# Kernel tuning notes

Measured on AMD Instinct MI355X. Metric: run time of the kernel, lower is better.

## Reference

```python
import jax, jax.numpy as jnp
import numpy as np

N_NODES = 50000
N_EDGES = 800000
D_IN = 128
D_HID = 128
N_CLASSES = 10


def gcn_conv(x, edge_index, edge_weight, W, b):
    """PyG GCNConv with edge weights: add self-loops, symmetric deg^-1/2 norm,
    gather-scale-scatter aggregation, then bias."""
    n = x.shape[0]
    row, col = edge_index[0], edge_index[1]
    loop = jnp.arange(n)
    row = jnp.concatenate([row, loop])
    col = jnp.concatenate([col, loop])
    ew = jnp.concatenate([edge_weight, jnp.ones((n,), edge_weight.dtype)])
    # degree computed at target nodes (source_to_target flow)
    deg = jax.ops.segment_sum(ew, col, num_segments=n)
    dinv = jnp.where(deg > 0, jax.lax.rsqrt(deg), 0.0)
    norm = dinv[row] * ew * dinv[col]  # [E+N]
    xw = x @ W  # [N, D_HID] dense GEMM first (PyG order)
    msgs = norm[:, None] * xw[row]  # [E+N, D_HID] edge-wise gather+scale
    out = jax.ops.segment_sum(msgs, col, num_segments=n)  # scatter-add
    return out + b


def setup_inputs() -> dict:
    key = jax.random.key(0)
    ks = jax.random.split(key, 9)
    x = jax.random.normal(ks[0], (N_NODES, D_IN), dtype=jnp.float32)
    edge_index = jax.random.randint(ks[1], (2, N_EDGES), 0, N_NODES, dtype=jnp.int64)
    edge_attr = jax.random.uniform(ks[2], (N_EDGES,), dtype=jnp.float32)
    s1 = 1.0 / np.sqrt(D_IN)
    s2 = 1.0 / np.sqrt(D_HID)
    W1 = jax.random.uniform(ks[3], (D_IN, D_HID), minval=-s1, maxval=s1, dtype=jnp.float32)
    b1 = jnp.zeros((D_HID,), jnp.float32)
    W2 = jax.random.uniform(ks[4], (D_HID, D_HID), minval=-s2, maxval=s2, dtype=jnp.float32)
    b2 = jnp.zeros((D_HID,), jnp.float32)
    Wm = jax.random.uniform(ks[5], (D_HID, N_CLASSES), minval=-s2, maxval=s2, dtype=jnp.float32)
    bm = jax.random.uniform(ks[6], (N_CLASSES,), minval=-s2, maxval=s2, dtype=jnp.float32)
    return {"x": x, "edge_index": edge_index, "edge_attr": edge_attr,
            "W1": W1, "b1": b1, "W2": W2, "b2": b2, "Wm": Wm, "bm": bm}


def reference(x, edge_index, edge_attr, W1, b1, W2, b2, Wm, bm):
    h = jax.nn.relu(gcn_conv(x, edge_index, edge_attr, W1, b1))
    h = jax.nn.relu(gcn_conv(h, edge_index, edge_attr, W2, b2))
    # F.dropout(training=False) is identity in eval mode
    g = jnp.mean(h, axis=0)  # [D_HID] graph readout
    return g @ Wm + bm  # [N_CLASSES]
```

## Files before the change

### kernel.cpp

```cpp
#include <hip/hip_runtime.h>

#define DD 128
#define CAP 8192

typedef __attribute__((ext_vector_type(8))) short short8v;
typedef __attribute__((ext_vector_type(4))) float float4v;

__device__ inline unsigned short f2b(float f) {
    unsigned int x = __float_as_uint(f);
    return (unsigned short)((x + 0x7fffu + ((x >> 16) & 1u)) >> 16);
}
__device__ inline float blo(unsigned int u) { return __uint_as_float(u << 16); }
__device__ inline float bhi(unsigned int u) { return __uint_as_float(u & 0xffff0000u); }

__global__ void wconv2_kernel(const float* __restrict__ W1, unsigned short* __restrict__ Wt1h,
                              unsigned short* __restrict__ Wt1l,
                              const float* __restrict__ W2, unsigned short* __restrict__ Wt2h,
                              unsigned short* __restrict__ Wt2l,
                              int* bcnt, int nb) {
    int t = threadIdx.x;
    if (blockIdx.x == 0 && t < nb) bcnt[t] = 0;
    int which = blockIdx.x >> 6;
    int idx = (blockIdx.x & 63) * 256 + t;
    int k = idx >> 7, nn = idx & 127;
    const float* W = which ? W2 : W1;
    unsigned short* Hh = which ? Wt2h : Wt1h;
    unsigned short* Hl = which ? Wt2l : Wt1l;
    float w = W[idx];
    unsigned short hi = f2b(w);
    float rem = w - __uint_as_float(((unsigned int)hi) << 16);
    Hh[nn * 128 + k] = hi;
    Hl[nn * 128 + k] = f2b(rem);
}

__global__ __launch_bounds__(256) void bin_direct_kernel(const int* __restrict__ row,
                                                         const int* __restrict__ col,
                                                         const float* __restrict__ ew,
                                                         int* bcnt, uint2* __restrict__ binned,
                                                         int E) {
    __shared__ int h[256];
    __shared__ int resv[256];
    int t = threadIdx.x;
    h[t] = 0;
    __syncthreads();
    int base = blockIdx.x * 2048;
    int myb[8], myrank[8];
    uint2 myrec[8];
    bool val[8];
#pragma unroll
    for (int j = 0; j < 8; ++j) {
        int e = base + j * 256 + t;
        val[j] = e < E;
        if (val[j]) {
            int c = col[e], r = row[e];
            myb[j] = c >> 8;
            myrank[j] = atomicAdd(&h[myb[j]], 1);
            myrec[j] = make_uint2(__float_as_uint(ew[e]),
                                  ((unsigned int)r << 8) | (unsigned int)(c & 255));
        }
    }
    __syncthreads();
    if (h[t]) resv[t] = atomicAdd(&bcnt[t], h[t]);
    __syncthreads();
#pragma unroll
    for (int j = 0; j < 8; ++j)
        if (val[j]) {
            int pos = resv[myb[j]] + myrank[j];
            if (pos < CAP) binned[(size_t)myb[j] * CAP + pos] = myrec[j];
        }
}

__global__ __launch_bounds__(256) void build_csr_kernel(const uint2* __restrict__ binned,
                                                        const int* __restrict__ bcnt,
                                                        uint2* __restrict__ startend,
                                                        float* __restrict__ dinv,
                                                        unsigned int* __restrict__ sedge, int n) {
    __shared__ unsigned int cnt[256];
    __shared__ unsigned int degf[256];
    __shared__ int sc[256];
    __shared__ int cur[256];
    int b = blockIdx.x, t = threadIdx.x;
    cnt[t] = 0; degf[t] = 0;
    __syncthreads();
    const int total = bcnt[b];
    const uint2* brec = binned + (size_t)b * CAP;
    for (int k = t; k < total; k += 256) {
        uint2 rec = brec[k];
        int cl = rec.y & 255;
        atomicAdd(&cnt[cl], 1u);
        atomicAdd(&degf[cl], (unsigned int)__float2uint_rn(__uint_as_float(rec.x) * 16777216.0f));
    }
    __syncthreads();
    int v = (int)cnt[t];
    sc[t] = v;
    __syncthreads();
    for (int off = 1; off < 256; off <<= 1) {
        int add = t >= off ? sc[t - off] : 0;
        __syncthreads();
        sc[t] += add;
        __syncthreads();
    }
    const int bstart = b * CAP;
    int myStart = bstart + sc[t] - v;
    cur[t] = myStart;
    int node = b * 256 + t;
    if (node < n) {
        startend[node] = make_uint2((unsigned int)myStart, (unsigned int)(myStart + v));
        float deg = 1.0f + (float)((double)degf[t] * (1.0 / 16777216.0));
        dinv[node] = 1.0f / sqrtf(deg);
    }
    __syncthreads();
    for (int k = t; k < total; k += 256) {
        uint2 rec = brec[k];
        int cl = rec.y & 255;
        int r = (int)(rec.y >> 8);
        int pos = atomicAdd(&cur[cl], 1);
        sedge[pos] = ((unsigned int)r << 16) | (unsigned int)f2b(__uint_as_float(rec.x));
    }
}

template <bool F32A>
__global__ __launch_bounds__(256) void mfma_gemm_kernel(const void* __restrict__ Av,
                                                        const unsigned short* __restrict__ WtHi,
                                                        const unsigned short* __restrict__ WtLo,
                                                        const float* __restrict__ dinv,
                                                        unsigned short* __restrict__ C, int n) {
    __shared__ __align__(16) unsigned short WLh[16 * 128 * 8];
    __shared__ __align__(16) unsigned short WLl[16 * 128 * 8];
    const int tid = threadIdx.x;

    for (int c = tid; c < 2048; c += 256) {
        int nn = c >> 4, k8 = c & 15;
        short8v vh = *(const short8v*)(WtHi + nn * 128 + k8 * 8);
        short8v vl = *(const short8v*)(WtLo + nn * 128 + k8 * 8);
        *(short8v*)(WLh + (k8 * 128 + nn) * 8) = vh;
        *(short8v*)(WLl + (k8 * 128 + nn) * 8) = vl;
    }
    __syncthreads();

    const int lane = tid & 63;
    const int l15 = lane & 15, l4 = lane >> 4;
    const int m0 = blockIdx.x * 128 + (tid >> 6) * 32;

    float4v acc[2][8];
#pragma unroll
    for (int i = 0; i < 2; ++i)
#pragma unroll
        for (int j = 0; j < 8; ++j) acc[i][j] = (float4v){0.f, 0.f, 0.f, 0.f};

#pragma unroll
    for (int kb = 0; kb < 4; ++kb) {
        short8v aF[2];
#pragma unroll
        for (int i = 0; i < 2; ++i) {
            int r = m0 + i * 16 + l15;
            r = r < n ? r : n - 1;
            if constexpr (F32A) {
                const float* xr = (const float*)Av + (size_t)r * 128 + kb * 32 + l4 * 8;
                float4 v0 = ((const float4*)xr)[0];
                float4 v1 = ((const float4*)xr)[1];
                short8v a;
                a[0] = (short)f2b(v0.x); a[1] = (short)f2b(v0.y);
                a[2] = (short)f2b(v0.z); a[3] = (short)f2b(v0.w);
                a[4] = (short)f2b(v1.x); a[5] = (short)f2b(v1.y);
                a[6] = (short)f2b(v1.z); a[7] = (short)f2b(v1.w);
                aF[i] = a;
            } else {
                aF[i] = *(const short8v*)((const unsigned short*)Av +
                                          (size_t)r * 128 + kb * 32 + l4 * 8);
            }
        }
        const int k8 = kb * 4 + l4;
#pragma unroll
        for (int j = 0; j < 8; ++j) {
            short8v bh = *(const short8v*)(WLh + (k8 * 128 + j * 16 + l15) * 8);
            short8v bl = *(const short8v*)(WLl + (k8 * 128 + j * 16 + l15) * 8);
            acc[0][j] = __builtin_amdgcn_mfma_f32_16x16x32_bf16(aF[0], bh, acc[0][j], 0, 0, 0);
            acc[1][j] = __builtin_amdgcn_mfma_f32_16x16x32_bf16(aF[1], bh, acc[1][j], 0, 0, 0);
            acc[0][j] = __builtin_amdgcn_mfma_f32_16x16x32_bf16(aF[0], bl, acc[0][j], 0, 0, 0);
            acc[1][j] = __builtin_amdgcn_mfma_f32_16x16x32_bf16(aF[1], bl, acc[1][j], 0, 0, 0);
        }
    }

#pragma unroll
    for (int i = 0; i < 2; ++i)
#pragma unroll
        for (int r = 0; r < 4; ++r) {
            int rr = m0 + i * 16 + l4 * 4 + r;
            if (rr < n) {
                float dvr = dinv[rr];
#pragma unroll
                for (int j = 0; j < 8; ++j)
                    C[(size_t)rr * 128 + j * 16 + l15] = f2b(acc[i][j][r] * dvr);
            }
        }
}

__device__ inline void agg_node_v4(int i, int sub, int q,
                                   const uint2* __restrict__ startend,
                                   const unsigned int* __restrict__ sedge,
                                   const float* __restrict__ dinv,
                                   const unsigned short* __restrict__ xw,
                                   const float* __restrict__ bias,
                                   float* __restrict__ a) {
#pragma unroll
    for (int j = 0; j < 8; ++j) a[j] = 0.f;
    const uint4* xw4 = (const uint4*)xw;
    uint2 se = startend[i];
    const int s = (int)se.x, e = (int)se.y;
    for (int k = s; k < e; k += 16) {
        unsigned int pe[4];
        uint4 u[4];
        float nv[4];
#pragma unroll
        for (int jj = 0; jj < 4; ++jj) {
            int idx = k + 4 * jj + sub;
            bool valid = idx < e;
            pe[jj] = sedge[valid ? idx : s];
            nv[jj] = valid ? __uint_as_float((pe[jj] & 0xffffu) << 16) : 0.f;
        }
#pragma unroll
        for (int jj = 0; jj < 4; ++jj)
            u[jj] = xw4[(size_t)(pe[jj] >> 16) * 16 + q];
#pragma unroll
        for (int jj = 0; jj < 4; ++jj) {
            a[0] += nv[jj] * blo(u[jj].x); a[1] += nv[jj] * bhi(u[jj].x);
            a[2] += nv[jj] * blo(u[jj].y); a[3] += nv[jj] * bhi(u[jj].y);
            a[4] += nv[jj] * blo(u[jj].z); a[5] += nv[jj] * bhi(u[jj].z);
            a[6] += nv[jj] * blo(u[jj].w); a[7] += nv[jj] * bhi(u[jj].w);
        }
    }
    if (sub == 0) {
        uint4 u = xw4[(size_t)i * 16 + q];
        a[0] += blo(u.x); a[1] += bhi(u.x);
        a[2] += blo(u.y); a[3] += bhi(u.y);
        a[4] += blo(u.z); a[5] += bhi(u.z);
        a[6] += blo(u.w); a[7] += bhi(u.w);
    }
#pragma unroll
    for (int j = 0; j < 8; ++j) {
        a[j] += __shfl_xor(a[j], 16);
        a[j] += __shfl_xor(a[j], 32);
    }
    const float dv = dinv[i];
    const float4 b0 = ((const float4*)bias)[q * 2];
    const float4 b1 = ((const float4*)bias)[q * 2 + 1];
    a[0] = fmaxf(dv * a[0] + b0.x, 0.f);
    a[1] = fmaxf(dv * a[1] + b0.y, 0.f);
    a[2] = fmaxf(dv * a[2] + b0.z, 0.f);
    a[3] = fmaxf(dv * a[3] + b0.w, 0.f);
    a[4] = fmaxf(dv * a[4] + b1.x, 0.f);
    a[5] = fmaxf(dv * a[5] + b1.y, 0.f);
    a[6] = fmaxf(dv * a[6] + b1.z, 0.f);
    a[7] = fmaxf(dv * a[7] + b1.w, 0.f);
}

__global__ __launch_bounds__(256) void agg_kernel(const uint2* __restrict__ startend,
                                                  const unsigned int* __restrict__ sedge,
                                                  const float* __restrict__ dinv,
                                                  const unsigned short* __restrict__ xw,
                                                  const float* __restrict__ bias,
                                                  unsigned short* __restrict__ h, int n) {
    const int i = blockIdx.x * 4 + (threadIdx.x >> 6);
    if (i >= n) return;
    const int lane = threadIdx.x & 63;
    const int sub = lane >> 4, q = lane & 15;
    float a[8];
    agg_node_v4(i, sub, q, startend, sedge, dinv, xw, bias, a);
    if (sub == 0) {
        uint4 o;
        o.x = (unsigned int)f2b(a[0]) | ((unsigned int)f2b(a[1]) << 16);
        o.y = (unsigned int)f2b(a[2]) | ((unsigned int)f2b(a[3]) << 16);
        o.z = (unsigned int)f2b(a[4]) | ((unsigned int)f2b(a[5]) << 16);
        o.w = (unsigned int)f2b(a[6]) | ((unsigned int)f2b(a[7]) << 16);
        ((uint4*)h)[(size_t)i * 16 + q] = o;
    }
}

__global__ __launch_bounds__(256) void agg_colsum_kernel(const uint2* __restrict__ startend,
                                                         const unsigned int* __restrict__ sedge,
                                                         const float* __restrict__ dinv,
                                                         const unsigned short* __restrict__ xw,
                                                         const float* __restrict__ bias,
                                                         float* __restrict__ partial, int n) {
    __shared__ float red[4][DD];
    const int w = threadIdx.x >> 6;
    const int lane = threadIdx.x & 63;
    const int sub = lane >> 4, q = lane & 15;
    const int i = blockIdx.x * 4 + w;
    float a[8];
#pragma unroll
    for (int j = 0; j < 8; ++j) a[j] = 0.f;
    if (i < n) agg_node_v4(i, sub, q, startend, sedge, dinv, xw, bias, a);
    if (sub == 0) {
#pragma unroll
        for (int j = 0; j < 8; ++j) red[w][q * 8 + j] = a[j];
    }
    __syncthreads();
    if (threadIdx.x < DD) {
        int f = threadIdx.x;
        float s = red[0][f] + red[1][f] + red[2][f] + red[3][f];
        partial[(size_t)blockIdx.x * DD + f] = s;
    }
}

__global__ __launch_bounds__(128) void colsum2_kernel(const float* __restrict__ partial,
                                                      float* __restrict__ partial2, int nblk) {
    int t = threadIdx.x;
    float acc = 0.f;
    for (int r = blockIdx.x; r < nblk; r += gridDim.x) acc += partial[(size_t)r * DD + t];
    partial2[blockIdx.x * DD + t] = acc;
}

__global__ void final_kernel(const float* __restrict__ partial2, const float* __restrict__ Wm,
                             const float* __restrict__ bm, float* __restrict__ out, int n) {
    __shared__ float g[DD];
    int t = threadIdx.x;
    float acc = 0.f;
    for (int b = 0; b < 512; ++b) acc += partial2[b * DD + t];
    g[t] = acc / (float)n;
    __syncthreads();
    if (t < 10) {
        float o = bm[t];
#pragma unroll
        for (int d = 0; d < DD; ++d) o += g[d] * Wm[d * 10 + t];
        out[t] = o;
    }
}

extern "C" void kernel_launch(void* const* d_in, const int* in_sizes, int n_in,
                              void* d_out, int out_size, void* d_ws, size_t ws_size,
                              hipStream_t stream) {
    const float* x  = (const float*)d_in[0];
    const int*   ei = (const int*)d_in[1];
    const float* ew = (const float*)d_in[2];
    const float* W1 = (const float*)d_in[3];
    const float* b1 = (const float*)d_in[4];
    const float* W2 = (const float*)d_in[5];
    const float* b2 = (const float*)d_in[6];
    const float* Wm = (const float*)d_in[7];
    const float* bm = (const float*)d_in[8];
    float* out = (float*)d_out;

    const int n = in_sizes[0] / DD;
    const int E = in_sizes[2];
    const int* row = ei;
    const int* col = ei + E;

    const int nb = (n + 255) >> 8;
    const int edgeChunks = (E + 2047) / 2048;
    const int aggBlocks = (n + 3) / 4;

    uint2* binned = (uint2*)d_ws;
    unsigned int* sedge = (unsigned int*)(binned + (size_t)nb * CAP);
    float* dinv    = (float*)(sedge + (size_t)nb * CAP);
    uint2* startend = (uint2*)(dinv + n);
    int*   bcnt    = (int*)(startend + n);
    float* partial = (float*)(bcnt + nb);
    float* partial2 = partial + (size_t)aggBlocks * DD;
    uintptr_t p = (uintptr_t)(partial2 + 512 * DD);
    p = (p + 15) & ~(uintptr_t)15;
    unsigned short* T0 = (unsigned short*)p;
    unsigned short* T1 = T0 + (size_t)n * DD;
    unsigned short* Wt1h = T1 + (size_t)n * DD;
    unsigned short* Wt1l = Wt1h + 16384;
    unsigned short* Wt2h = Wt1l + 16384;
    unsigned short* Wt2l = Wt2h + 16384;

    wconv2_kernel<<<128, 256, 0, stream>>>(W1, Wt1h, Wt1l, W2, Wt2h, Wt2l, bcnt, nb);

    bin_direct_kernel<<<edgeChunks, 256, 0, stream>>>(row, col, ew, bcnt, binned, E);
    build_csr_kernel<<<nb, 256, 0, stream>>>(binned, bcnt, startend, dinv, sedge, n);

    const int gemmBlocks = (n + 127) / 128;

    mfma_gemm_kernel<true><<<gemmBlocks, 256, 0, stream>>>(x, Wt1h, Wt1l, dinv, T0, n);
    agg_kernel<<<aggBlocks, 256, 0, stream>>>(startend, sedge, dinv, T0, b1, T1, n);

    mfma_gemm_kernel<false><<<gemmBlocks, 256, 0, stream>>>(T1, Wt2h, Wt2l, dinv, T0, n);
    agg_colsum_kernel<<<aggBlocks, 256, 0, stream>>>(startend, sedge, dinv, T0, b2, partial, n);

    colsum2_kernel<<<512, 128, 0, stream>>>(partial, partial2, aggBlocks);
    final_kernel<<<1, 128, 0, stream>>>(partial2, Wm, bm, out, n);
}
```

Baseline: 163.9 us.

## Merge prep kernels and overlap CSR placement with first GEMM

Binning and weight conversion now run as block roles of one kernel, and the bcnt zeroing moves to a memset. CSR construction is split so the edge placement pass runs as extra blocks alongside the first GEMM. The colsum2 grid also shrinks from 512 to 128 blocks. The aim is to cut launch count and let placement overlap GEMM work, at the cost of an added memset call and of shared-memory usage that is sized for the larger role.

Measured after the change: 174.7 us. 1.07x slower.

```diff
diff --git a/kernel.cpp b/kernel.cpp
--- a/kernel.cpp
+++ b/kernel.cpp
@@ -13,15 +13,15 @@
 __device__ inline float blo(unsigned int u) { return __uint_as_float(u << 16); }
 __device__ inline float bhi(unsigned int u) { return __uint_as_float(u & 0xffff0000u); }
 
-__global__ void wconv2_kernel(const float* __restrict__ W1, unsigned short* __restrict__ Wt1h,
-                              unsigned short* __restrict__ Wt1l,
-                              const float* __restrict__ W2, unsigned short* __restrict__ Wt2h,
-                              unsigned short* __restrict__ Wt2l,
-                              int* bcnt, int nb) {
+__device__ inline void wconv_role(int wb, const float* __restrict__ W1,
+                                  unsigned short* __restrict__ Wt1h,
+                                  unsigned short* __restrict__ Wt1l,
+                                  const float* __restrict__ W2,
+                                  unsigned short* __restrict__ Wt2h,
+                                  unsigned short* __restrict__ Wt2l) {
     int t = threadIdx.x;
-    if (blockIdx.x == 0 && t < nb) bcnt[t] = 0;
-    int which = blockIdx.x >> 6;
-    int idx = (blockIdx.x & 63) * 256 + t;
+    int which = wb >> 6;
+    int idx = (wb & 63) * 256 + t;
     int k = idx >> 7, nn = idx & 127;
     const float* W = which ? W2 : W1;
     unsigned short* Hh = which ? Wt2h : Wt1h;
@@ -33,17 +33,15 @@
     Hl[nn * 128 + k] = f2b(rem);
 }
 
-__global__ __launch_bounds__(256) void bin_direct_kernel(const int* __restrict__ row,
-                                                         const int* __restrict__ col,
-                                                         const float* __restrict__ ew,
-                                                         int* bcnt, uint2* __restrict__ binned,
-                                                         int E) {
+__device__ inline void bin_role(int bid, const int* __restrict__ row,
+                                const int* __restrict__ col, const float* __restrict__ ew,
+                                int* bcnt, uint2* __restrict__ binned, int E) {
     __shared__ int h[256];
     __shared__ int resv[256];
     int t = threadIdx.x;
     h[t] = 0;
     __syncthreads();
-    int base = blockIdx.x * 2048;
+    int base = bid * 2048;
     int myb[8], myrank[8];
     uint2 myrec[8];
     bool val[8];
@@ -70,15 +68,28 @@
         }
 }
 
-__global__ __launch_bounds__(256) void build_csr_kernel(const uint2* __restrict__ binned,
-                                                        const int* __restrict__ bcnt,
-                                                        uint2* __restrict__ startend,
-                                                        float* __restrict__ dinv,
-                                                        unsigned int* __restrict__ sedge, int n) {
+__global__ __launch_bounds__(256) void prep_kernel(const int* __restrict__ row,
+                                                   const int* __restrict__ col,
+                                                   const float* __restrict__ ew,
+                                                   int* bcnt, uint2* __restrict__ binned, int E,
+                                                   int edgeChunks,
+                                                   const float* __restrict__ W1,
+                                                   unsigned short* Wt1h, unsigned short* Wt1l,
+                                                   const float* __restrict__ W2,
+                                                   unsigned short* Wt2h, unsigned short* Wt2l) {
+    if ((int)blockIdx.x < edgeChunks)
+        bin_role(blockIdx.x, row, col, ew, bcnt, binned, E);
+    else
+        wconv_role(blockIdx.x - edgeChunks, W1, Wt1h, Wt1l, W2, Wt2h, Wt2l);
+}
+
+__global__ __launch_bounds__(256) void phase1_kernel(const uint2* __restrict__ binned,
+                                                     const int* __restrict__ bcnt,
+                                                     uint2* __restrict__ startend,
+                                                     float* __restrict__ dinv, int n) {
     __shared__ unsigned int cnt[256];
     __shared__ unsigned int degf[256];
     __shared__ int sc[256];
-    __shared__ int cur[256];
     int b = blockIdx.x, t = threadIdx.x;
     cnt[t] = 0; degf[t] = 0;
     __syncthreads();
@@ -100,16 +111,26 @@
         sc[t] += add;
         __syncthreads();
     }
-    const int bstart = b * CAP;
-    int myStart = bstart + sc[t] - v;
-    cur[t] = myStart;
+    int myStart = b * CAP + sc[t] - v;
     int node = b * 256 + t;
     if (node < n) {
         startend[node] = make_uint2((unsigned int)myStart, (unsigned int)(myStart + v));
         float deg = 1.0f + (float)((double)degf[t] * (1.0 / 16777216.0));
         dinv[node] = 1.0f / sqrtf(deg);
     }
-    __syncthreads();
+}
+
+__device__ inline void place_role(int b, const uint2* __restrict__ binned,
+                                  const int* __restrict__ bcnt,
+                                  const uint2* __restrict__ startend,
+                                  unsigned int* __restrict__ sedge, int n) {
+    __shared__ int cur[256];
+    int t = threadIdx.x;
+    int node = b * 256 + t;
+    cur[t] = node < n ? (int)startend[node].x : 0;
+    __syncthreads();
+    const int total = bcnt[b];
+    const uint2* brec = binned + (size_t)b * CAP;
     for (int k = t; k < total; k += 256) {
         uint2 rec = brec[k];
         int cl = rec.y & 255;
@@ -120,11 +141,11 @@
 }
 
 template <bool F32A>
-__global__ __launch_bounds__(256) void mfma_gemm_kernel(const void* __restrict__ Av,
-                                                        const unsigned short* __restrict__ WtHi,
-                                                        const unsigned short* __restrict__ WtLo,
-                                                        const float* __restrict__ dinv,
-                                                        unsigned short* __restrict__ C, int n) {
+__device__ inline void gemm_body(int bid, const void* __restrict__ Av,
+                                 const unsigned short* __restrict__ WtHi,
+                                 const unsigned short* __restrict__ WtLo,
+                                 const float* __restrict__ dinv,
+                                 unsigned short* __restrict__ C, int n) {
     __shared__ __align__(16) unsigned short WLh[16 * 128 * 8];
     __shared__ __align__(16) unsigned short WLl[16 * 128 * 8];
     const int tid = threadIdx.x;
@@ -140,7 +161,7 @@
 
     const int lane = tid & 63;
     const int l15 = lane & 15, l4 = lane >> 4;
-    const int m0 = blockIdx.x * 128 + (tid >> 6) * 32;
+    const int m0 = bid * 128 + (tid >> 6) * 32;
 
     float4v acc[2][8];
 #pragma unroll
@@ -194,6 +215,30 @@
                     C[(size_t)rr * 128 + j * 16 + l15] = f2b(acc[i][j][r] * dvr);
             }
         }
+}
+
+__global__ __launch_bounds__(256) void gemm1_place_kernel(const float* __restrict__ x,
+                                                          const unsigned short* __restrict__ Wt1h,
+                                                          const unsigned short* __restrict__ Wt1l,
+                                                          const float* __restrict__ dinv,
+                                                          unsigned short* __restrict__ T0, int n,
+                                                          int gemmBlocks,
+                                                          const uint2* __restrict__ binned,
+                                                          const int* __restrict__ bcnt,
+                                                          const uint2* __restrict__ startend,
+                                                          unsigned int* __restrict__ sedge) {
+    if ((int)blockIdx.x < gemmBlocks)
+        gemm_body<true>(blockIdx.x, x, Wt1h, Wt1l, dinv, T0, n);
+    else
+        place_role(blockIdx.x - gemmBlocks, binned, bcnt, startend, sedge, n);
+}
+
+__global__ __launch_bounds__(256) void mfma_gemm2_kernel(const unsigned short* __restrict__ A,
+                                                         const unsigned short* __restrict__ WtHi,
+                                                         const unsigned short* __restrict__ WtLo,
+                                                         const float* __restrict__ dinv,
+                                                         unsigned short* __restrict__ C, int n) {
+    gemm_body<false>(blockIdx.x, A, WtHi, WtLo, dinv, C, n);
 }
 
 __device__ inline void agg_node_v4(int i, int sub, int q,
@@ -317,7 +362,7 @@
     __shared__ float g[DD];
     int t = threadIdx.x;
     float acc = 0.f;
-    for (int b = 0; b < 512; ++b) acc += partial2[b * DD + t];
+    for (int b = 0; b < 128; ++b) acc += partial2[b * DD + t];
     g[t] = acc / (float)n;
     __syncthreads();
     if (t < 10) {
@@ -350,6 +395,7 @@
     const int nb = (n + 255) >> 8;
     const int edgeChunks = (E + 2047) / 2048;
     const int aggBlocks = (n + 3) / 4;
+    const int gemmBlocks = (n + 127) / 128;
 
     uint2* binned = (uint2*)d_ws;
     unsigned int* sedge = (unsigned int*)(binned + (size_t)nb * CAP);
@@ -358,7 +404,7 @@
     int*   bcnt    = (int*)(startend + n);
     float* partial = (float*)(bcnt + nb);
     float* partial2 = partial + (size_t)aggBlocks * DD;
-    uintptr_t p = (uintptr_t)(partial2 + 512 * DD);
+    uintptr_t p = (uintptr_t)(partial2 + 128 * DD);
     p = (p + 15) & ~(uintptr_t)15;
     unsigned short* T0 = (unsigned short*)p;
     unsigned short* T1 = T0 + (size_t)n * DD;
@@ -367,19 +413,22 @@
     unsigned short* Wt2h = Wt1l + 16384;
     unsigned short* Wt2l = Wt2h + 16384;
 
-    wconv2_kernel<<<128, 256, 0, stream>>>(W1, Wt1h, Wt1l, W2, Wt2h, Wt2l, bcnt, nb);
-
-    bin_direct_kernel<<<edgeChunks, 256, 0, stream>>>(row, col, ew, bcnt, binned, E);
-    build_csr_kernel<<<nb, 256, 0, stream>>>(binned, bcnt, startend, dinv, sedge, n);
-
-    const int gemmBlocks = (n + 127) / 128;
-
-    mfma_gemm_kernel<true><<<gemmBlocks, 256, 0, stream>>>(x, Wt1h, Wt1l, dinv, T0, n);
+    hipMemsetAsync(bcnt, 0, nb * sizeof(int), stream);
+
+    prep_kernel<<<edgeChunks + 128, 256, 0, stream>>>(row, col, ew, bcnt, binned, E, edgeChunks,
+                                                      W1, Wt1h, Wt1l, W2, Wt2h, Wt2l);
+
+    phase1_kernel<<<nb, 256, 0, stream>>>(binned, bcnt, startend, dinv, n);
+
+    gemm1_place_kernel<<<gemmBlocks + nb, 256, 0, stream>>>(x, Wt1h, Wt1l, dinv, T0, n,
+                                                            gemmBlocks, binned, bcnt,
+                                                            startend, sedge);
+
     agg_kernel<<<aggBlocks, 256, 0, stream>>>(startend, sedge, dinv, T0, b1, T1, n);
 
-    mfma_gemm_kernel<false><<<gemmBlocks, 256, 0, stream>>>(T1, Wt2h, Wt2l, dinv, T0, n);
+    mfma_gemm2_kernel<<<gemmBlocks, 256, 0, stream>>>(T1, Wt2h, Wt2l, dinv, T0, n);
     agg_colsum_kernel<<<aggBlocks, 256, 0, stream>>>(startend, sedge, dinv, T0, b2, partial, n);
 
-    colsum2_kernel<<<512, 128, 0, stream>>>(partial, partial2, aggBlocks);
+    colsum2_kernel<<<128, 128, 0, stream>>>(partial, partial2, aggBlocks);
     final_kernel<<<1, 128, 0, stream>>>(partial2, Wm, bm, out, n);
 }
```
